# Performance work log

Hardware: AMD Instinct MI355X
Metric: run time of the kernel (lower is better)

The kernel has to match this reference:

```python
import jax, jax.numpy as jnp
import numpy as np

N_NODES = 100000
N_EDGES = 1600000
IN_CH = 64
HID = 64
OUT_CH = 1


def setup_inputs() -> dict:
    key = jax.random.key(0)
    ks = jax.random.split(key, 6)
    x = jax.random.normal(ks[0], (N_NODES, IN_CH), dtype=jnp.float32)
    edge_index = jax.random.randint(ks[1], (2, N_EDGES), 0, N_NODES, dtype=jnp.int64)
    edge_weight = jax.random.uniform(ks[2], (N_EDGES,), dtype=jnp.float32)
    W1 = jax.random.normal(ks[3], (IN_CH, HID), dtype=jnp.float32) / np.sqrt(IN_CH)
    b1 = jnp.zeros((HID,), dtype=jnp.float32)
    W2 = jax.random.normal(ks[4], (HID, OUT_CH), dtype=jnp.float32) / np.sqrt(HID)
    b2 = jnp.zeros((OUT_CH,), dtype=jnp.float32)
    return {"x": x, "edge_index": edge_index, "edge_weight": edge_weight,
            "W1": W1, "b1": b1, "W2": W2, "b2": b2}


def _gcn_conv(x, row, col, ew, W, b, n_nodes):
    # PyG GCNConv: add self-loops (weight 1), symmetric deg normalization,
    # linear (no bias) -> message x_j * norm -> sum at target -> + bias.
    loop = jnp.arange(n_nodes, dtype=row.dtype)
    r = jnp.concatenate([row, loop])
    c = jnp.concatenate([col, loop])
    w = jnp.concatenate([ew, jnp.ones((n_nodes,), dtype=ew.dtype)])
    deg = jax.ops.segment_sum(w, c, num_segments=n_nodes)  # [N]
    dinv = jnp.where(deg > 0, jax.lax.rsqrt(deg), 0.0)
    norm = dinv[r] * w * dinv[c]  # [E+N]
    h = x @ W  # [N, out]
    msg = h[r] * norm[:, None]  # [E+N, out] gather
    out = jax.ops.segment_sum(msg, c, num_segments=n_nodes)  # scatter-add
    return out + b


def reference(x, edge_index, edge_weight, W1, b1, W2, b2):
    row, col = edge_index[0], edge_index[1]
    n = x.shape[0]
    h = _gcn_conv(x, row, col, edge_weight, W1, b1, n)
    h = jax.nn.relu(h)
    out = _gcn_conv(h, row, col, edge_weight, W2, b2, n)
    return out
```

## Files before the change

kernel.cpp:

```cpp
#include <hip/hip_runtime.h>


#define N_NODES 100000
#define N_EDGES 1600000
#define CNT_SHIFT 42
#define SUM_MASK ((1ull << CNT_SHIFT) - 1)
#define BSZ 256
#define NBUCK 391
#define NB1 512
#define EPB 3125

typedef _Float16 half2v __attribute__((ext_vector_type(2)));

__global__ void p1_hist(const int* __restrict__ idx, int* __restrict__ hist) {
    __shared__ int h[NBUCK];
    int t = threadIdx.x, blk = blockIdx.x;
    for (int i = t; i < NBUCK; i += 256) h[i] = 0;
    __syncthreads();
    int e0 = blk * EPB;
    for (int i = t; i < EPB; i += 256) {
        int c = idx[N_EDGES + e0 + i];
        atomicAdd(&h[c >> 8], 1);
    }
    __syncthreads();
    for (int i = t; i < NBUCK; i += 256) hist[(size_t)i * NB1 + blk] = h[i];
}

__global__ void p2a_scan(int* __restrict__ hist, int* __restrict__ btot) {
    __shared__ int s[NB1];
    int t = threadIdx.x, b = blockIdx.x;
    int v = hist[(size_t)b * NB1 + t];
    s[t] = v;
    __syncthreads();
#pragma unroll
    for (int d = 1; d < NB1; d <<= 1) {
        int u = (t >= d) ? s[t - d] : 0;
        __syncthreads();
        s[t] += u;
        __syncthreads();
    }
    hist[(size_t)b * NB1 + t] = s[t] - v;
    if (t == NB1 - 1) btot[b] = s[NB1 - 1];
}

__global__ void p3_part(const int* __restrict__ idx, const float* __restrict__ w,
                        const int* __restrict__ hist, const int* __restrict__ btot,
                        float2* __restrict__ bin) {
    __shared__ int sc[512];
    __shared__ int base[NBUCK];
    __shared__ int h[NBUCK];
    int t = threadIdx.x, blk = blockIdx.x;
    int v = (t < NBUCK) ? btot[t] : 0;
    sc[t] = v;
    __syncthreads();
#pragma unroll
    for (int d = 1; d < 512; d <<= 1) {
        int u = (t >= d) ? sc[t - d] : 0;
        __syncthreads();
        sc[t] += u;
        __syncthreads();
    }
    if (t < NBUCK) {
        base[t] = sc[t] - v + hist[(size_t)t * NB1 + blk];
        h[t] = 0;
    }
    __syncthreads();
    int e0 = blk * EPB;
    for (int i = t; i < EPB; i += 512) {
        int e = e0 + i;
        int r = idx[e];
        int c = idx[N_EDGES + e];
        int b = c >> 8;
        int lr = atomicAdd(&h[b], 1);
        bin[base[b] + lr] = make_float2(__int_as_float(r | ((c & 255) << 17)), w[e]);
    }
}

__global__ void p4_build(const float2* __restrict__ bin, const int* __restrict__ btot,
                         int* __restrict__ off, float* __restrict__ dinv,
                         float2* __restrict__ pairs) {
    __shared__ int sc[512];
    __shared__ unsigned long long pk[BSZ];
    __shared__ float dl[BSZ];
    __shared__ int ofl[BSZ];
    __shared__ int rk[BSZ];
    int t = threadIdx.x, b = blockIdx.x;
    int v = (t < NBUCK) ? btot[t] : 0;
    sc[t] = v;
    if (t < BSZ) { pk[t] = 0ull; rk[t] = 0; }
    __syncthreads();
#pragma unroll
    for (int d = 1; d < 512; d <<= 1) {
        int u = (t >= d) ? sc[t - d] : 0;
        __syncthreads();
        sc[t] += u;
        __syncthreads();
    }
    int s0 = (b > 0) ? sc[b - 1] : 0;
    int s1 = sc[b];
    for (int j = s0 + t; j < s1; j += 512) {
        float2 p = bin[j];
        int cl = (__float_as_int(p.x) >> 17) & 255;
        unsigned long long add =
            (1ull << CNT_SHIFT) | (unsigned long long)(p.y * 4294967296.0f);
        atomicAdd(&pk[cl], add);
    }
    __syncthreads();
    unsigned long long pv = 0;
    int c = 0;
    if (t < BSZ) {
        pv = pk[t];
        c = (int)(pv >> CNT_SHIFT);
        sc[t] = c;
    }
    __syncthreads();
#pragma unroll
    for (int d = 1; d < BSZ; d <<= 1) {
        int u = (t >= d && t < BSZ) ? sc[t - d] : 0;
        __syncthreads();
        if (t < BSZ) sc[t] += u;
        __syncthreads();
    }
    if (t < BSZ) {
        int o = s0 + sc[t] - c;
        ofl[t] = o;
        float deg = 1.0f + (float)(pv & SUM_MASK) * 2.3283064365386963e-10f;
        float di = rsqrtf(deg);
        dl[t] = di;
        int node = b * BSZ + t;
        if (node < N_NODES) { off[node] = o; dinv[node] = di; }
    }
    if (b == NBUCK - 1 && t == 0) off[N_NODES] = s1;
    __syncthreads();
    for (int j = s0 + t; j < s1; j += 512) {
        float2 p = bin[j];
        int bits = __float_as_int(p.x);
        int r = bits & 0x1FFFF;
        int cl = (bits >> 17) & 255;
        int rank = atomicAdd(&rk[cl], 1);
        pairs[ofl[cl] + rank] = make_float2(__int_as_float(r), p.y * dl[cl]);
    }
}

__global__ void gemm1(const float* __restrict__ x, const float* __restrict__ W1,
                      const float* __restrict__ dinv, _Float16* __restrict__ h1) {
    __shared__ float xs[128 * 68];
    __shared__ float w1s[64 * 64];
    int t = threadIdx.x;
    int row0 = blockIdx.x * 128;

    const float4* W4g = (const float4*)W1;
    float4* w1s4 = (float4*)w1s;
#pragma unroll
    for (int i = 0; i < 8; i++) w1s4[t + 128 * i] = W4g[t + 128 * i];
    const float4* X4 = (const float4*)x;
#pragma unroll
    for (int i = 0; i < 16; i++) {
        int fi = t + 128 * i;
        int rl = fi >> 4;
        int kq = fi & 15;
        int row = row0 + rl;
        float4 vv = (row < N_NODES) ? X4[(size_t)row * 16 + kq]
                                    : make_float4(0.f, 0.f, 0.f, 0.f);
        *(float4*)&xs[rl * 68 + kq * 4] = vv;
    }
    __syncthreads();

    int cq = t & 7;
    int rq = t >> 3;
    float acc[8][8];
#pragma unroll
    for (int i = 0; i < 8; i++)
#pragma unroll
        for (int j = 0; j < 8; j++) acc[i][j] = 0.f;

    for (int k = 0; k < 64; k += 4) {
        float4 xv[8];
#pragma unroll
        for (int i = 0; i < 8; i++)
            xv[i] = *(const float4*)&xs[(rq + 16 * i) * 68 + k];
        float4 wv[4][2];
#pragma unroll
        for (int kk = 0; kk < 4; kk++) {
            wv[kk][0] = w1s4[(k + kk) * 16 + 2 * cq];
            wv[kk][1] = w1s4[(k + kk) * 16 + 2 * cq + 1];
        }
#pragma unroll
        for (int i = 0; i < 8; i++) {
            float xk[4] = {xv[i].x, xv[i].y, xv[i].z, xv[i].w};
#pragma unroll
            for (int kk = 0; kk < 4; kk++) {
                acc[i][0] += xk[kk] * wv[kk][0].x;
                acc[i][1] += xk[kk] * wv[kk][0].y;
                acc[i][2] += xk[kk] * wv[kk][0].z;
                acc[i][3] += xk[kk] * wv[kk][0].w;
                acc[i][4] += xk[kk] * wv[kk][1].x;
                acc[i][5] += xk[kk] * wv[kk][1].y;
                acc[i][6] += xk[kk] * wv[kk][1].z;
                acc[i][7] += xk[kk] * wv[kk][1].w;
            }
        }
    }
#pragma unroll
    for (int i = 0; i < 8; i++) {
        int row = row0 + rq + 16 * i;
        if (row < N_NODES) {
            float di = dinv[row];
            half2v h4[4];
#pragma unroll
            for (int j = 0; j < 4; j++)
                h4[j] = half2v{(_Float16)(acc[i][2 * j] * di),
                               (_Float16)(acc[i][2 * j + 1] * di)};
            *(float4*)(h1 + (size_t)row * 64 + 8 * cq) = *(float4*)h4;
        }
    }
}

__global__ void gather1(const half2v* __restrict__ h1v, const float2* __restrict__ pairs,
                        const int* __restrict__ off, const float* __restrict__ dinv,
                        const float* __restrict__ b1, const float* __restrict__ W2,
                        const float* __restrict__ b2, float* __restrict__ h2,
                        float* __restrict__ out, int n) {
    int t = threadIdx.x;
    int lane = t & 63;
    int half = lane >> 5;
    int cl = lane & 31;
    int dst = blockIdx.x * 2 + (t >> 6);
    if (dst >= n) return;
    int beg = off[dst];
    int end = off[dst + 1];
    float di = dinv[dst];
    float a0 = 0.f, a1 = 0.f, b0 = 0.f, b1a = 0.f;
    float c0 = 0.f, c1 = 0.f, d0 = 0.f, d1 = 0.f;
    int j = beg + half;
    for (; j + 14 < end; j += 16) {
        float2 p0 = pairs[j],      p1 = pairs[j + 2],  p2 = pairs[j + 4],  p3 = pairs[j + 6];
        float2 p4 = pairs[j + 8],  p5 = pairs[j + 10], p6 = pairs[j + 12], p7 = pairs[j + 14];
        half2v v0 = h1v[__float_as_int(p0.x) * 32 + cl];
        half2v v1 = h1v[__float_as_int(p1.x) * 32 + cl];
        half2v v2 = h1v[__float_as_int(p2.x) * 32 + cl];
        half2v v3 = h1v[__float_as_int(p3.x) * 32 + cl];
        half2v v4 = h1v[__float_as_int(p4.x) * 32 + cl];
        half2v v5 = h1v[__float_as_int(p5.x) * 32 + cl];
        half2v v6 = h1v[__float_as_int(p6.x) * 32 + cl];
        half2v v7 = h1v[__float_as_int(p7.x) * 32 + cl];
        a0 += p0.y * (float)v0[0]; a1 += p0.y * (float)v0[1];
        b0 += p1.y * (float)v1[0]; b1a += p1.y * (float)v1[1];
        c0 += p2.y * (float)v2[0]; c1 += p2.y * (float)v2[1];
        d0 += p3.y * (float)v3[0]; d1 += p3.y * (float)v3[1];
        a0 += p4.y * (float)v4[0]; a1 += p4.y * (float)v4[1];
        b0 += p5.y * (float)v5[0]; b1a += p5.y * (float)v5[1];
        c0 += p6.y * (float)v6[0]; c1 += p6.y * (float)v6[1];
        d0 += p7.y * (float)v7[0]; d1 += p7.y * (float)v7[1];
    }
    for (; j + 6 < end; j += 8) {
        float2 p0 = pairs[j], p1 = pairs[j + 2], p2 = pairs[j + 4], p3 = pairs[j + 6];
        half2v v0 = h1v[__float_as_int(p0.x) * 32 + cl];
        half2v v1 = h1v[__float_as_int(p1.x) * 32 + cl];
        half2v v2 = h1v[__float_as_int(p2.x) * 32 + cl];
        half2v v3 = h1v[__float_as_int(p3.x) * 32 + cl];
        a0 += p0.y * (float)v0[0]; a1 += p0.y * (float)v0[1];
        b0 += p1.y * (float)v1[0]; b1a += p1.y * (float)v1[1];
        c0 += p2.y * (float)v2[0]; c1 += p2.y * (float)v2[1];
        d0 += p3.y * (float)v3[0]; d1 += p3.y * (float)v3[1];
    }
    for (; j < end; j += 2) {
        float2 p = pairs[j];
        half2v v = h1v[__float_as_int(p.x) * 32 + cl];
        a0 += p.y * (float)v[0]; a1 += p.y * (float)v[1];
    }
    float t0 = (a0 + b0) + (c0 + d0);
    float t1 = (a1 + b1a) + (c1 + d1);
    t0 += __shfl_xor(t0, 32, 64);
    t1 += __shfl_xor(t1, 32, 64);
    half2v sv = h1v[dst * 32 + cl];
    t0 += (float)sv[0] * di;
    t1 += (float)sv[1] * di;
    float2 b1p = ((const float2*)b1)[cl];
    float v0 = fmaxf(t0 + b1p.x, 0.0f);
    float v1 = fmaxf(t1 + b1p.y, 0.0f);
    float2 w2p = ((const float2*)W2)[cl];
    float p = v0 * w2p.x + v1 * w2p.y;
#pragma unroll
    for (int o = 16; o > 0; o >>= 1) p += __shfl_xor(p, o, 64);
    if (lane == 0) {
        h2[dst] = p * di;
        out[dst] = b2[0] + p * di * di;
    }
}

__global__ void gather2(const float2* __restrict__ pairs, const int* __restrict__ off,
                        const float* __restrict__ h2, float* __restrict__ out, int n) {
    int t = threadIdx.x;
    int i = blockIdx.x * 64 + (t >> 2);
    if (i >= n) return;
    int q = t & 3;
    int beg = off[i], end = off[i + 1];
    float s = 0.f;
    for (int j = beg + q; j < end; j += 4) {
        float2 p = pairs[j];
        s += p.y * h2[__float_as_int(p.x)];
    }
    s += __shfl_xor(s, 1, 64);
    s += __shfl_xor(s, 2, 64);
    if (q == 0) out[i] += s;
}

extern "C" void kernel_launch(void* const* d_in, const int* in_sizes, int n_in,
                              void* d_out, int out_size, void* d_ws, size_t ws_size,
                              hipStream_t stream) {
    const float* x   = (const float*)d_in[0];
    const int*   idx = (const int*)d_in[1];
    const float* ew  = (const float*)d_in[2];
    const float* W1  = (const float*)d_in[3];
    const float* b1  = (const float*)d_in[4];
    const float* W2  = (const float*)d_in[5];
    const float* b2  = (const float*)d_in[6];
    float* out = (float*)d_out;

    const int N = N_NODES;

    float* ws = (float*)d_ws;
    int*    off  = (int*)ws;
    float*  dinv = ws + 100004;
    int*    btot = (int*)(ws + 200004);
    int*    hist = (int*)(ws + 200400);
    float2* bin  = (float2*)(ws + 200400 + 200192);
    _Float16* h1 = (_Float16*)(ws + 200400);
    float2* pairs = (float2*)(ws + 3600592);
    float*  h2   = ws + 6800592;

    p1_hist<<<NB1, 256, 0, stream>>>(idx, hist);
    p2a_scan<<<NBUCK, NB1, 0, stream>>>(hist, btot);
    p3_part<<<NB1, 512, 0, stream>>>(idx, ew, hist, btot, bin);
    p4_build<<<NBUCK, 512, 0, stream>>>(bin, btot, off, dinv, pairs);
    gemm1<<<(N + 127) / 128, 128, 0, stream>>>(x, W1, dinv, h1);
    gather1<<<(N + 1) / 2, 128, 0, stream>>>((const half2v*)h1, pairs, off, dinv,
                                             b1, W2, b2, h2, out, N);
    gather2<<<(N + 63) / 64, 256, 0, stream>>>(pairs, off, h2, out, N);
}
```

Baseline: 226.3 us.

## Split h1 into four channel-slice planes and gather per slice with partial combine

gemm1 now writes h1 as four planes of 16 fp16 channels each, instead of rows of 64. gather1 launches separate blocks per slice, and each wave handles 8 edges at a time across 8 channel lanes, so each slice plane (about 3.2MB) is more likely to stay resident in L2/Infinity Cache while it is gathered. A new combine kernel sums the four slice partials and writes h2 and out. The trade-off is that edge pairs and offsets are now read four times, partial sums make an extra global round trip, and there is one more kernel launch.

```diff
diff --git a/kernel.cpp b/kernel.cpp
--- a/kernel.cpp
+++ b/kernel.cpp
@@ -201,6 +201,7 @@
             }
         }
     }
+    int slice = cq >> 1;
 #pragma unroll
     for (int i = 0; i < 8; i++) {
         int row = row0 + rq + 16 * i;
@@ -211,7 +212,8 @@
             for (int j = 0; j < 4; j++)
                 h4[j] = half2v{(_Float16)(acc[i][2 * j] * di),
                                (_Float16)(acc[i][2 * j + 1] * di)};
-            *(float4*)(h1 + (size_t)row * 64 + 8 * cq) = *(float4*)h4;
+            *(float4*)(h1 + ((size_t)slice * N_NODES + row) * 16 + (cq & 1) * 8) =
+                *(float4*)h4;
         }
     }
 }
@@ -219,74 +221,64 @@
 __global__ void gather1(const half2v* __restrict__ h1v, const float2* __restrict__ pairs,
                         const int* __restrict__ off, const float* __restrict__ dinv,
                         const float* __restrict__ b1, const float* __restrict__ W2,
+                        float* __restrict__ part, int n) {
+    int t = threadIdx.x;
+    int lane = t & 63;
+    int e = lane >> 3;
+    int c = lane & 7;
+    int s = blockIdx.x & 3;
+    int grp = blockIdx.x >> 2;
+    int wid = t >> 6;
+    const half2v* plane = h1v + (size_t)s * N_NODES * 8;
+    float2 b1p = ((const float2*)b1)[s * 8 + c];
+    float2 w2p = ((const float2*)W2)[s * 8 + c];
+#pragma unroll
+    for (int dd = 0; dd < 4; dd++) {
+        int dst = grp * 16 + wid * 4 + dd;
+        if (dst >= n) return;
+        int beg = off[dst], end = off[dst + 1];
+        float di = dinv[dst];
+        float a0 = 0.f, a1 = 0.f;
+        for (int j = beg; j < end; j += 8) {
+            int je = j + e;
+            float2 p;
+            if (je < end) {
+                unsigned long long u =
+                    __builtin_nontemporal_load((const unsigned long long*)(pairs + je));
+                p.x = __int_as_float((int)(u & 0xFFFFFFFFull));
+                p.y = __int_as_float((int)(u >> 32));
+            } else {
+                p = make_float2(__int_as_float(dst), 0.f);
+            }
+            half2v v = plane[(size_t)__float_as_int(p.x) * 8 + c];
+            a0 += p.y * (float)v[0];
+            a1 += p.y * (float)v[1];
+        }
+        a0 += __shfl_xor(a0, 8, 64);  a1 += __shfl_xor(a1, 8, 64);
+        a0 += __shfl_xor(a0, 16, 64); a1 += __shfl_xor(a1, 16, 64);
+        a0 += __shfl_xor(a0, 32, 64); a1 += __shfl_xor(a1, 32, 64);
+        half2v sv = plane[(size_t)dst * 8 + c];
+        a0 += (float)sv[0] * di;
+        a1 += (float)sv[1] * di;
+        float v0 = fmaxf(a0 + b1p.x, 0.0f);
+        float v1 = fmaxf(a1 + b1p.y, 0.0f);
+        float p = v0 * w2p.x + v1 * w2p.y;
+        p += __shfl_xor(p, 1, 64);
+        p += __shfl_xor(p, 2, 64);
+        p += __shfl_xor(p, 4, 64);
+        if (lane == 0) part[(size_t)s * n + dst] = p;
+    }
+}
+
+__global__ void combine(const float* __restrict__ part, const float* __restrict__ dinv,
                         const float* __restrict__ b2, float* __restrict__ h2,
                         float* __restrict__ out, int n) {
-    int t = threadIdx.x;
-    int lane = t & 63;
-    int half = lane >> 5;
-    int cl = lane & 31;
-    int dst = blockIdx.x * 2 + (t >> 6);
-    if (dst >= n) return;
-    int beg = off[dst];
-    int end = off[dst + 1];
-    float di = dinv[dst];
-    float a0 = 0.f, a1 = 0.f, b0 = 0.f, b1a = 0.f;
-    float c0 = 0.f, c1 = 0.f, d0 = 0.f, d1 = 0.f;
-    int j = beg + half;
-    for (; j + 14 < end; j += 16) {
-        float2 p0 = pairs[j],      p1 = pairs[j + 2],  p2 = pairs[j + 4],  p3 = pairs[j + 6];
-        float2 p4 = pairs[j + 8],  p5 = pairs[j + 10], p6 = pairs[j + 12], p7 = pairs[j + 14];
-        half2v v0 = h1v[__float_as_int(p0.x) * 32 + cl];
-        half2v v1 = h1v[__float_as_int(p1.x) * 32 + cl];
-        half2v v2 = h1v[__float_as_int(p2.x) * 32 + cl];
-        half2v v3 = h1v[__float_as_int(p3.x) * 32 + cl];
-        half2v v4 = h1v[__float_as_int(p4.x) * 32 + cl];
-        half2v v5 = h1v[__float_as_int(p5.x) * 32 + cl];
-        half2v v6 = h1v[__float_as_int(p6.x) * 32 + cl];
-        half2v v7 = h1v[__float_as_int(p7.x) * 32 + cl];
-        a0 += p0.y * (float)v0[0]; a1 += p0.y * (float)v0[1];
-        b0 += p1.y * (float)v1[0]; b1a += p1.y * (float)v1[1];
-        c0 += p2.y * (float)v2[0]; c1 += p2.y * (float)v2[1];
-        d0 += p3.y * (float)v3[0]; d1 += p3.y * (float)v3[1];
-        a0 += p4.y * (float)v4[0]; a1 += p4.y * (float)v4[1];
-        b0 += p5.y * (float)v5[0]; b1a += p5.y * (float)v5[1];
-        c0 += p6.y * (float)v6[0]; c1 += p6.y * (float)v6[1];
-        d0 += p7.y * (float)v7[0]; d1 += p7.y * (float)v7[1];
-    }
-    for (; j + 6 < end; j += 8) {
-        float2 p0 = pairs[j], p1 = pairs[j + 2], p2 = pairs[j + 4], p3 = pairs[j + 6];
-        half2v v0 = h1v[__float_as_int(p0.x) * 32 + cl];
-        half2v v1 = h1v[__float_as_int(p1.x) * 32 + cl];
-        half2v v2 = h1v[__float_as_int(p2.x) * 32 + cl];
-        half2v v3 = h1v[__float_as_int(p3.x) * 32 + cl];
-        a0 += p0.y * (float)v0[0]; a1 += p0.y * (float)v0[1];
-        b0 += p1.y * (float)v1[0]; b1a += p1.y * (float)v1[1];
-        c0 += p2.y * (float)v2[0]; c1 += p2.y * (float)v2[1];
-        d0 += p3.y * (float)v3[0]; d1 += p3.y * (float)v3[1];
-    }
-    for (; j < end; j += 2) {
-        float2 p = pairs[j];
-        half2v v = h1v[__float_as_int(p.x) * 32 + cl];
-        a0 += p.y * (float)v[0]; a1 += p.y * (float)v[1];
-    }
-    float t0 = (a0 + b0) + (c0 + d0);
-    float t1 = (a1 + b1a) + (c1 + d1);
-    t0 += __shfl_xor(t0, 32, 64);
-    t1 += __shfl_xor(t1, 32, 64);
-    half2v sv = h1v[dst * 32 + cl];
-    t0 += (float)sv[0] * di;
-    t1 += (float)sv[1] * di;
-    float2 b1p = ((const float2*)b1)[cl];
-    float v0 = fmaxf(t0 + b1p.x, 0.0f);
-    float v1 = fmaxf(t1 + b1p.y, 0.0f);
-    float2 w2p = ((const float2*)W2)[cl];
-    float p = v0 * w2p.x + v1 * w2p.y;
-#pragma unroll
-    for (int o = 16; o > 0; o >>= 1) p += __shfl_xor(p, o, 64);
-    if (lane == 0) {
-        h2[dst] = p * di;
-        out[dst] = b2[0] + p * di * di;
-    }
+    int i = blockIdx.x * 256 + threadIdx.x;
+    if (i >= n) return;
+    float p = part[i] + part[n + i] + part[2 * (size_t)n + i] + part[3 * (size_t)n + i];
+    float di = dinv[i];
+    h2[i] = p * di;
+    out[i] = b2[0] + p * di * di;
 }
 
 __global__ void gather2(const float2* __restrict__ pairs, const int* __restrict__ off,
@@ -329,13 +321,15 @@
     _Float16* h1 = (_Float16*)(ws + 200400);
     float2* pairs = (float2*)(ws + 3600592);
     float*  h2   = ws + 6800592;
+    float*  part = ws + 6900592;
 
     p1_hist<<<NB1, 256, 0, stream>>>(idx, hist);
     p2a_scan<<<NBUCK, NB1, 0, stream>>>(hist, btot);
     p3_part<<<NB1, 512, 0, stream>>>(idx, ew, hist, btot, bin);
     p4_build<<<NBUCK, 512, 0, stream>>>(bin, btot, off, dinv, pairs);
     gemm1<<<(N + 127) / 128, 128, 0, stream>>>(x, W1, dinv, h1);
-    gather1<<<(N + 1) / 2, 128, 0, stream>>>((const half2v*)h1, pairs, off, dinv,
-                                             b1, W2, b2, h2, out, N);
+    gather1<<<4 * ((N + 15) / 16), 256, 0, stream>>>((const half2v*)h1, pairs, off,
+                                                     dinv, b1, W2, part, N);
+    combine<<<(N + 255) / 256, 256, 0, stream>>>(part, dinv, b2, h2, out, N);
     gather2<<<(N + 63) / 64, 256, 0, stream>>>(pairs, off, h2, out, N);
 }
```

Result: slower. 342.2 us (+51.2%).
